# Optimization experiments

Hardware: AMD Instinct MI355X
Metric: run time of the kernel (lower is better)

Reference implementation:

```python
import jax, jax.numpy as jnp
import numpy as np

CUTOFF = 4          # lattice cutoff radius (module init arg)
NMAX = 64           # padded max neighbors per mobile site (~58 actual at cutoff=4)
BATCH = 131072      # number of independent configurations
B_SOFT = 0.01       # softening constant b in vint
FAR = 1e6           # padding position, masked out


def _rot(c):
    return np.array([[np.cos(c), -np.sin(c)], [np.sin(c), np.cos(c)]])


def _build_geometry():
    """Replicates PotEnergy1P.__init__ (with the intended, bug-fixed math)."""
    s3 = np.sqrt(3.0)
    base = [np.array([0.5, s3 / 6]), np.array([1.0, -s3 / 3]),
            np.array([1.5, s3 / 6]), np.array([1.0, 2 * s3 / 3])]
    mobile = base \
        + [_rot(2 * np.pi / 3) @ p for p in base] \
        + [_rot(4 * np.pi / 3) @ p for p in base]
    mobile = np.stack(mobile)                      # [12, 2]

    def ntopos(n1, n2):
        return np.array([0.5, s3 / 6]) + n1 * np.array([1.0, 0.0]) \
            + n2 * np.array([-0.5, s3 / 2])

    rng = range(-4 * CUTOFF, 4 * CUTOFF)
    grid = np.array([ntopos(n1, n2) for n1 in rng for n2 in rng])  # [G, 2]
    dist = np.linalg.norm(grid[:, None, :] - mobile[None, :, :], axis=-1)  # [G, 12]
    not_mobile = ~np.any(np.isclose(dist, 0.0, atol=1e-8), axis=1)        # [G]

    neighbors = np.full((12, NMAX, 2), FAR, dtype=np.float32)
    mask = np.zeros((12, NMAX), dtype=np.float32)
    for i in range(12):
        idx = np.where(not_mobile & (dist[:, i] < CUTOFF))[0]
        k = len(idx)
        assert k <= NMAX
        neighbors[i, :k] = grid[idx]
        mask[i, :k] = 1.0
    return neighbors, mask


def setup_inputs() -> dict:
    key = jax.random.key(0)
    x = jax.random.normal(key, (BATCH, 24), dtype=jnp.float32)
    neighbors, mask = _build_geometry()
    return {"x": x,
            "neighbors": jnp.asarray(neighbors),
            "mask": jnp.asarray(mask)}


def reference(x, neighbors, mask):
    # x: [B, 24] -> [B, 12, 2] mobile positions
    xr = x.reshape(x.shape[0], -1, 2)
    # pairwise displacement to all padded neighbors: [B, 12, NMAX, 2]
    d = xr[:, :, None, :] - neighbors[None, :, :, :]
    r = jnp.sqrt(jnp.sum(d * d, axis=-1))          # [B, 12, NMAX]
    v = jnp.exp(-r) / (r + B_SOFT)                 # vint with a=1.0, b=0.01
    return jnp.sum(v * mask[None], axis=(1, 2))    # [B] total potential energy
```

## Files before the change

kernel.cpp:

```cpp
#include <hip/hip_runtime.h>
#include <math.h>

#define NMAX   64
#define NSITES 12
#define BLOCK  256
#define EPB    64
#define RS     68

#define B_SOFT 0.01f
#define PAD_C  14.0f
#define TBL_LO 1392
#define TBL_N  800
#define RAW_LO (TBL_LO * 8)

#define NB_F   (NSITES * RS)
#define GW_NBX (2 * TBL_N)
#define GW_NBY (GW_NBX + NB_F)
#define GW_F   (GW_NBY + NB_F)

#define L_NBX  (2 * TBL_N)
#define L_NBY  (L_NBX + NB_F)
#define L_PART (L_NBY + NB_F)
#define SMEM_F (L_PART + 3 * EPB)

__device__ __align__(16) float g_ws[GW_F];
__device__ int g_mq[4];

typedef float v2f __attribute__((ext_vector_type(2)));
typedef float v4f __attribute__((ext_vector_type(4)));

__device__ __forceinline__ float f_exact(float r2) {
    const float r = sqrtf(r2);
    return expf(-r) / (r + B_SOFT);
}

__global__ void init_kernel(const float* __restrict__ neighbors,
                            const float* __restrict__ mask) {
    __shared__ int cnt[NSITES];
    const int tid  = threadIdx.x;
    const int wv   = tid >> 6;
    const int lane = tid & 63;

    for (int i = tid; i < TBL_N; i += BLOCK) {
        const unsigned ii = (unsigned)(i + TBL_LO);
        const float b0 = __builtin_bit_cast(float, ii << 19);
        const float b1 = __builtin_bit_cast(float, (ii + 1u) << 19);
        const float f0 = f_exact(b0);
        const float f1 = f_exact(b1);
        const float fm = f_exact(0.5f * (b0 + b1));
        const float sl = (f1 - f0) / (b1 - b0);
        const float c  = f0 - sl * b0 - 0.5f * (0.5f * (f0 + f1) - fm);
        g_ws[2 * i]     = c;
        g_ws[2 * i + 1] = sl;
    }

    for (int i = tid; i < 2 * NB_F; i += BLOCK) g_ws[GW_NBX + i] = PAD_C;
    __syncthreads();

    for (int s = wv; s < NSITES; s += 4) {
        const bool keep = mask[s * NMAX + lane] > 0.5f;
        const unsigned long long bal = __ballot(keep);
        if (keep) {
            const int pos = __popcll(bal & ((1ull << lane) - 1ull));
            const float2 p = ((const float2*)neighbors)[s * NMAX + lane];
            g_ws[GW_NBX + s * RS + pos] = p.x;
            g_ws[GW_NBY + s * RS + pos] = p.y;
        }
        if (lane == 0) cnt[s] = __popcll(bal);
    }
    __syncthreads();
    if (tid < 4) {
        const int mm = max(cnt[3 * tid],
                       max(cnt[3 * tid + 1], cnt[3 * tid + 2]));
        g_mq[tid] = (mm + 3) & ~3;
    }
}

__global__ __launch_bounds__(BLOCK, 8)
void pot_energy_kernel(const float* __restrict__ x,
                       float* __restrict__ out, int B) {
    __shared__ __align__(16) float smem[SMEM_F];
    const int tid  = threadIdx.x;
    const int w    = tid >> 6;
    const int lane = tid & 63;

    {
        const float4* s4 = (const float4*)g_ws;
        float4* d4 = (float4*)smem;
        #pragma unroll
        for (int i0 = 0; i0 < 4; ++i0) {
            const int i = tid + i0 * BLOCK;
            if (i < GW_F / 4) d4[i] = s4[i];
        }
    }
    const int q = __builtin_amdgcn_readfirstlane(w);
    const int m = g_mq[q];
    __syncthreads();

    const int e  = blockIdx.x * EPB + lane;
    const int el = (e < B) ? e : 0;

    const float* xb = x + (size_t)el * 24 + q * 6;
    const float2 pa = ((const float2*)xb)[0];
    const float2 pb = ((const float2*)xb)[1];
    const float2 pc = ((const float2*)xb)[2];
    const float xs_[3] = { pa.x, pb.x, pc.x };
    const float ys_[3] = { pa.y, pb.y, pc.y };

    const char* tb = (const char*)smem - RAW_LO;
    const v2f eps2 = { 9.094947e-13f, 9.094947e-13f };

    float accC = 0.f, accS = 0.f;
    #pragma unroll
    for (int s = 0; s < 3; ++s) {
        const int site = q * 3 + s;
        const float* __restrict__ rx = smem + L_NBX + site * RS;
        const float* __restrict__ ry = smem + L_NBY + site * RS;
        const v2f xs2 = { xs_[s], xs_[s] };
        const v2f ys2 = { ys_[s], ys_[s] };
        #pragma unroll 2
        for (int j0 = 0; j0 < m; j0 += 4) {
            const v4f nx4 = *(const v4f*)(rx + j0);
            const v4f ny4 = *(const v4f*)(ry + j0);
            const v2f dxA = xs2 - nx4.xy;
            const v2f dxB = xs2 - nx4.zw;
            const v2f dyA = ys2 - ny4.xy;
            const v2f dyB = ys2 - ny4.zw;
            const v2f r2A = __builtin_elementwise_fma(
                dyA, dyA, __builtin_elementwise_fma(dxA, dxA, eps2));
            const v2f r2B = __builtin_elementwise_fma(
                dyB, dyB, __builtin_elementwise_fma(dxB, dxB, eps2));
            const float r2k[4] = { r2A.x, r2A.y, r2B.x, r2B.y };
            #pragma unroll
            for (int k = 0; k < 4; ++k) {
                const unsigned raw =
                    (__builtin_bit_cast(unsigned, r2k[k]) >> 16) & 0xFFF8u;
                const float2 cs = *(const float2*)(tb + raw);
                accC += cs.x;
                accS = fmaf(cs.y, r2k[k], accS);
            }
        }
    }

    const float av = accC + accS;
    if (w != 0) smem[L_PART + (w - 1) * EPB + lane] = av;
    __syncthreads();
    if (w == 0 && e < B) {
        out[e] = av + smem[L_PART + lane]
                    + smem[L_PART + EPB + lane]
                    + smem[L_PART + 2 * EPB + lane];
    }
}

extern "C" void kernel_launch(void* const* d_in, const int* in_sizes, int n_in,
                              void* d_out, int out_size, void* d_ws, size_t ws_size,
                              hipStream_t stream) {
    const float* x   = (const float*)d_in[0];
    const float* nbr = (const float*)d_in[1];
    const float* msk = (const float*)d_in[2];
    float* out = (float*)d_out;

    const int B = in_sizes[0] / 24;

    init_kernel<<<1, BLOCK, 0, stream>>>(nbr, msk);

    const int blocks = (B + EPB - 1) / EPB;
    pot_energy_kernel<<<blocks, BLOCK, 0, stream>>>(x, out, B);
}
```

Measured before the change: 80.65 us.

## Use finer piecewise-constant r² lookup table and larger blocks

Replaces the 800-entry linear-interpolation table (intercept plus slope per bin) with a 6400-entry piecewise-constant table indexed by more mantissa bits of r². Each neighbor pair then needs a single 32-bit LDS read and an add instead of a 64-bit read plus an FMA. The init kernel that builds the table is spread over 26 blocks. The main kernel moves to 1024-thread blocks, each handling 256 configurations, with launch bounds of 2 blocks per CU. In exchange, accuracy depends on a step-function approximation, and each block uses more LDS.

```diff
diff --git a/kernel.cpp b/kernel.cpp
--- a/kernel.cpp
+++ b/kernel.cpp
@@ -3,22 +3,21 @@
 
 #define NMAX   64
 #define NSITES 12
-#define BLOCK  256
-#define EPB    64
+#define BLOCK  1024
+#define EPB    256
 #define RS     68
 
 #define B_SOFT 0.01f
 #define PAD_C  14.0f
-#define TBL_LO 1392
-#define TBL_N  800
-#define RAW_LO (TBL_LO * 8)
+#define R2_BASE_BITS 0x2B800000u
+#define TBL_N  6400
 
 #define NB_F   (NSITES * RS)
-#define GW_NBX (2 * TBL_N)
+#define GW_NBX TBL_N
 #define GW_NBY (GW_NBX + NB_F)
 #define GW_F   (GW_NBY + NB_F)
 
-#define L_NBX  (2 * TBL_N)
+#define L_NBX  TBL_N
 #define L_NBY  (L_NBX + NB_F)
 #define L_PART (L_NBY + NB_F)
 #define SMEM_F (L_PART + 3 * EPB)
@@ -34,49 +33,48 @@
     return expf(-r) / (r + B_SOFT);
 }
 
+#define INIT_BLOCKS 26
+
 __global__ void init_kernel(const float* __restrict__ neighbors,
                             const float* __restrict__ mask) {
-    __shared__ int cnt[NSITES];
-    const int tid  = threadIdx.x;
-    const int wv   = tid >> 6;
-    const int lane = tid & 63;
+    const int tid = threadIdx.x;
+    const int gid = blockIdx.x * 256 + tid;
 
-    for (int i = tid; i < TBL_N; i += BLOCK) {
-        const unsigned ii = (unsigned)(i + TBL_LO);
-        const float b0 = __builtin_bit_cast(float, ii << 19);
-        const float b1 = __builtin_bit_cast(float, (ii + 1u) << 19);
-        const float f0 = f_exact(b0);
-        const float f1 = f_exact(b1);
-        const float fm = f_exact(0.5f * (b0 + b1));
-        const float sl = (f1 - f0) / (b1 - b0);
-        const float c  = f0 - sl * b0 - 0.5f * (0.5f * (f0 + f1) - fm);
-        g_ws[2 * i]     = c;
-        g_ws[2 * i + 1] = sl;
+    if (gid < TBL_N) {
+        const unsigned b0 = R2_BASE_BITS + ((unsigned)gid << 16);
+        const unsigned b1 = b0 + (1u << 16);
+        const float f0 = f_exact(__builtin_bit_cast(float, b0));
+        const float f1 = f_exact(__builtin_bit_cast(float, b1));
+        g_ws[gid] = 0.5f * (f0 + f1);
     }
 
-    for (int i = tid; i < 2 * NB_F; i += BLOCK) g_ws[GW_NBX + i] = PAD_C;
-    __syncthreads();
+    if (blockIdx.x == 0) {
+        __shared__ int cnt[NSITES];
+        const int wv = tid >> 6, lane = tid & 63;
+        for (int i = tid; i < 2 * NB_F; i += 256) g_ws[GW_NBX + i] = PAD_C;
+        __syncthreads();
 
-    for (int s = wv; s < NSITES; s += 4) {
-        const bool keep = mask[s * NMAX + lane] > 0.5f;
-        const unsigned long long bal = __ballot(keep);
-        if (keep) {
-            const int pos = __popcll(bal & ((1ull << lane) - 1ull));
-            const float2 p = ((const float2*)neighbors)[s * NMAX + lane];
-            g_ws[GW_NBX + s * RS + pos] = p.x;
-            g_ws[GW_NBY + s * RS + pos] = p.y;
+        for (int s = wv; s < NSITES; s += 4) {
+            const bool keep = mask[s * NMAX + lane] > 0.5f;
+            const unsigned long long bal = __ballot(keep);
+            if (keep) {
+                const int pos = __popcll(bal & ((1ull << lane) - 1ull));
+                const float2 p = ((const float2*)neighbors)[s * NMAX + lane];
+                g_ws[GW_NBX + s * RS + pos] = p.x;
+                g_ws[GW_NBY + s * RS + pos] = p.y;
+            }
+            if (lane == 0) cnt[s] = __popcll(bal);
         }
-        if (lane == 0) cnt[s] = __popcll(bal);
-    }
-    __syncthreads();
-    if (tid < 4) {
-        const int mm = max(cnt[3 * tid],
-                       max(cnt[3 * tid + 1], cnt[3 * tid + 2]));
-        g_mq[tid] = (mm + 3) & ~3;
+        __syncthreads();
+        if (tid < 4) {
+            const int mm = max(cnt[3 * tid],
+                           max(cnt[3 * tid + 1], cnt[3 * tid + 2]));
+            g_mq[tid] = (mm + 3) & ~3;
+        }
     }
 }
 
-__global__ __launch_bounds__(BLOCK, 8)
+__global__ __launch_bounds__(BLOCK, 2)
 void pot_energy_kernel(const float* __restrict__ x,
                        float* __restrict__ out, int B) {
     __shared__ __align__(16) float smem[SMEM_F];
@@ -88,16 +86,17 @@
         const float4* s4 = (const float4*)g_ws;
         float4* d4 = (float4*)smem;
         #pragma unroll
-        for (int i0 = 0; i0 < 4; ++i0) {
+        for (int i0 = 0; i0 < 2; ++i0) {
             const int i = tid + i0 * BLOCK;
             if (i < GW_F / 4) d4[i] = s4[i];
         }
     }
-    const int q = __builtin_amdgcn_readfirstlane(w);
+    const int q = __builtin_amdgcn_readfirstlane(w & 3);
     const int m = g_mq[q];
     __syncthreads();
 
-    const int e  = blockIdx.x * EPB + lane;
+    const int eb = ((w >> 2) << 6) + lane;
+    const int e  = blockIdx.x * EPB + eb;
     const int el = (e < B) ? e : 0;
 
     const float* xb = x + (size_t)el * 24 + q * 6;
@@ -107,10 +106,10 @@
     const float xs_[3] = { pa.x, pb.x, pc.x };
     const float ys_[3] = { pa.y, pb.y, pc.y };
 
-    const char* tb = (const char*)smem - RAW_LO;
+    const char* tbl = (const char*)smem;
     const v2f eps2 = { 9.094947e-13f, 9.094947e-13f };
 
-    float accC = 0.f, accS = 0.f;
+    float acc0 = 0.f, acc1 = 0.f;
     #pragma unroll
     for (int s = 0; s < 3; ++s) {
         const int site = q * 3 + s;
@@ -133,22 +132,22 @@
             const float r2k[4] = { r2A.x, r2A.y, r2B.x, r2B.y };
             #pragma unroll
             for (int k = 0; k < 4; ++k) {
-                const unsigned raw =
-                    (__builtin_bit_cast(unsigned, r2k[k]) >> 16) & 0xFFF8u;
-                const float2 cs = *(const float2*)(tb + raw);
-                accC += cs.x;
-                accS = fmaf(cs.y, r2k[k], accS);
+                const unsigned bits = __builtin_bit_cast(unsigned, r2k[k]);
+                const unsigned off  = ((bits >> 14) & ~3u)
+                                      - (R2_BASE_BITS >> 14);
+                const float c = *(const float*)(tbl + off);
+                if (k & 1) acc1 += c; else acc0 += c;
             }
         }
     }
 
-    const float av = accC + accS;
-    if (w != 0) smem[L_PART + (w - 1) * EPB + lane] = av;
+    const float av = acc0 + acc1;
+    if (q != 0) smem[L_PART + (q - 1) * EPB + eb] = av;
     __syncthreads();
-    if (w == 0 && e < B) {
-        out[e] = av + smem[L_PART + lane]
-                    + smem[L_PART + EPB + lane]
-                    + smem[L_PART + 2 * EPB + lane];
+    if (q == 0 && e < B) {
+        out[e] = av + smem[L_PART + eb]
+                    + smem[L_PART + EPB + eb]
+                    + smem[L_PART + 2 * EPB + eb];
     }
 }
 
@@ -162,7 +161,7 @@
 
     const int B = in_sizes[0] / 24;
 
-    init_kernel<<<1, BLOCK, 0, stream>>>(nbr, msk);
+    init_kernel<<<INIT_BLOCKS, 256, 0, stream>>>(nbr, msk);
 
     const int blocks = (B + EPB - 1) / EPB;
     pot_energy_kernel<<<blocks, BLOCK, 0, stream>>>(x, out, B);
```

New measurement: 83.92 us. +4.1%, slower.
